# Optimization experiments

Hardware: AMD Instinct MI355X
Metric: run time of the kernel (lower is better)

Reference implementation:

```python
import jax, jax.numpy as jnp
import numpy as np

THRESHOLD = 2.0 / 3.0


def _quantize_1_58_bit(weight):
    """BitNet b1.58: ternary {-1,0,+1} * scale, scale = mean(|w|) clamped."""
    scale = jnp.clip(jnp.mean(jnp.abs(weight)), 1e-5, 1000.0)
    weight_norm = jnp.clip(weight / scale, -10.0, 10.0)
    q = jnp.where(weight_norm > THRESHOLD, 1.0,
                  jnp.where(weight_norm < -THRESHOLD, -1.0, 0.0)).astype(weight.dtype)
    return q, scale


def setup_inputs() -> dict:
    key = jax.random.key(0)
    k1, k2 = jax.random.split(key)
    B, S, D_IN, D_OUT = 4, 2048, 4096, 4096
    x = jax.random.normal(k1, (B, S, D_IN), dtype=jnp.float32)
    weight = jax.random.normal(k2, (D_OUT, D_IN), dtype=jnp.float32)
    bias = jnp.zeros((D_OUT,), dtype=jnp.float32)
    return {"x": x, "weight": weight, "bias": bias}


def reference(x, weight, bias):
    # Training-path forward value == eval-path forward value:
    # dequantized ternary weight, F.linear semantics (x @ W.T + b).
    q, scale = _quantize_1_58_bit(weight)
    weight_q = q * scale  # [out, in]
    out = jnp.einsum('bsi,oi->bso', x, weight_q) + bias
    return out
```

## Files before the change

kernel.cpp:

```cpp
#include <hip/hip_runtime.h>
#include <hip/hip_bf16.h>
#include <stdint.h>


#define BM 128
#define BN 128
#define BK 64

typedef __bf16 bf16x8 __attribute__((ext_vector_type(8)));
typedef float f32x4 __attribute__((ext_vector_type(4)));
typedef unsigned short u16x8 __attribute__((ext_vector_type(8)));

__device__ __forceinline__ unsigned short f2bf_rne(float f) {
  union { float f; unsigned int u; } v; v.f = f;
  unsigned int u = v.u;
  u += 0x7FFFu + ((u >> 16) & 1u);
  return (unsigned short)(u >> 16);
}

__global__ void absum_kernel(const float4* __restrict__ w, int n4,
                             double* __restrict__ out) {
  float s = 0.f;
  for (int i = blockIdx.x * blockDim.x + threadIdx.x; i < n4;
       i += gridDim.x * blockDim.x) {
    float4 v = w[i];
    s += fabsf(v.x) + fabsf(v.y) + fabsf(v.z) + fabsf(v.w);
  }
#pragma unroll
  for (int off = 32; off > 0; off >>= 1) s += __shfl_down(s, off);
  __shared__ float partial[4];
  if ((threadIdx.x & 63) == 0) partial[threadIdx.x >> 6] = s;
  __syncthreads();
  if (threadIdx.x == 0)
    atomicAdd(out, (double)(partial[0] + partial[1] + partial[2] + partial[3]));
}

__global__ void quant_kernel(const float4* __restrict__ w, int n8,
                             const double* __restrict__ sum, double inv_cnt,
                             u16x8* __restrict__ q) {
  float scale = (float)fmin(fmax(sum[0] * inv_cnt, 1e-5), 1000.0);
  const float T = 2.0f / 3.0f;
  for (int i = blockIdx.x * blockDim.x + threadIdx.x; i < n8;
       i += gridDim.x * blockDim.x) {
    float4 a = w[2 * i], b = w[2 * i + 1];
    float f[8] = {a.x, a.y, a.z, a.w, b.x, b.y, b.z, b.w};
    u16x8 o;
#pragma unroll
    for (int j = 0; j < 8; ++j) {
      float n = f[j] / scale;
      o[j] = (n > T) ? 0x3F80u : ((n < -T) ? 0xBF80u : 0u);
    }
    q[i] = o;
  }
}

__global__ void xcvt_kernel(const float4* __restrict__ x, int n8,
                            u16x8* __restrict__ xb) {
  for (int i = blockIdx.x * blockDim.x + threadIdx.x; i < n8;
       i += gridDim.x * blockDim.x) {
    float4 a = x[2 * i], b = x[2 * i + 1];
    float f[8] = {a.x, a.y, a.z, a.w, b.x, b.y, b.z, b.w};
    u16x8 o;
#pragma unroll
    for (int j = 0; j < 8; ++j) o[j] = f2bf_rne(f[j]);
    xb[i] = o;
  }
}

__global__ void gemm_kernel(const ushort* __restrict__ xb,
                            const ushort* __restrict__ qb,
                            const float* __restrict__ bias,
                            const double* __restrict__ sum,
                            float* __restrict__ out,
                            int M, int N, int K, double inv_cnt) {
  __shared__ __align__(16) ushort As[BM * BK];
  __shared__ __align__(16) ushort Bs[BN * BK];

  const int t = threadIdx.x;
  const int wave = t >> 6;
  const int lane = t & 63;
  const int m0 = blockIdx.y * BM;
  const int n0 = blockIdx.x * BN;

  const int wr = (wave >> 1) * 64;
  const int wc = (wave & 1) * 64;
  const int lm = lane & 15;
  const int lk = lane >> 4;

  const int srow = lane >> 3;
  const int schunk = (lane & 7) ^ srow;
  const ushort* ag = xb + (size_t)(m0 + wave * 32 + srow) * K + schunk * 8;
  const ushort* bg = qb + (size_t)(n0 + wave * 32 + srow) * K + schunk * 8;
  ushort* al = &As[(wave * 32) * BK];
  ushort* bl = &Bs[(wave * 32) * BK];

  f32x4 acc[4][4] = {};

  for (int k0 = 0; k0 < K; k0 += BK) {
#pragma unroll
    for (int s = 0; s < 4; ++s) {
      __builtin_amdgcn_global_load_lds(
          (const __attribute__((address_space(1))) void*)(ag + (size_t)s * 8 * K),
          (__attribute__((address_space(3))) void*)(al + s * 8 * BK), 16, 0, 0);
      __builtin_amdgcn_global_load_lds(
          (const __attribute__((address_space(1))) void*)(bg + (size_t)s * 8 * K),
          (__attribute__((address_space(3))) void*)(bl + s * 8 * BK), 16, 0, 0);
    }
    __syncthreads();

#pragma unroll
    for (int ks = 0; ks < 2; ++ks) {
      bf16x8 af[4], bf[4];
#pragma unroll
      for (int i = 0; i < 4; ++i) {
        const int row = wr + i * 16 + lm;
        const int slot = (ks * 4 + lk) ^ (lm & 7);
        af[i] = *(const bf16x8*)&As[row * BK + slot * 8];
      }
#pragma unroll
      for (int j = 0; j < 4; ++j) {
        const int row = wc + j * 16 + lm;
        const int slot = (ks * 4 + lk) ^ (lm & 7);
        bf[j] = *(const bf16x8*)&Bs[row * BK + slot * 8];
      }
#pragma unroll
      for (int i = 0; i < 4; ++i)
#pragma unroll
        for (int j = 0; j < 4; ++j)
          acc[i][j] = __builtin_amdgcn_mfma_f32_16x16x32_bf16(af[i], bf[j],
                                                             acc[i][j], 0, 0, 0);
    }
    __syncthreads();
    ag += BK;
    bg += BK;
  }

  float scale = (float)fmin(fmax(sum[0] * inv_cnt, 1e-5), 1000.0);

#pragma unroll
  for (int j = 0; j < 4; ++j) {
    const int col = n0 + wc + j * 16 + lm;
    const float bv = bias[col];
#pragma unroll
    for (int i = 0; i < 4; ++i) {
      const int row = m0 + wr + i * 16 + lk * 4;
      float* op = out + (size_t)row * N + col;
#pragma unroll
      for (int r = 0; r < 4; ++r)
        op[(size_t)r * N] = acc[i][j][r] * scale + bv;
    }
  }
}

extern "C" void kernel_launch(void* const* d_in, const int* in_sizes, int n_in,
                              void* d_out, int out_size, void* d_ws,
                              size_t ws_size, hipStream_t stream) {
  const float* x = (const float*)d_in[0];
  const float* w = (const float*)d_in[1];
  const float* bias = (const float*)d_in[2];
  float* out = (float*)d_out;

  const int DOUT = in_sizes[2];
  const int DIN = in_sizes[1] / DOUT;
  const int M = in_sizes[0] / DIN;
  const int N = DOUT, K = DIN;

  char* ws = (char*)d_ws;
  double* sum = (double*)ws;
  ushort* xb = (ushort*)(ws + 256);
  ushort* qb = (ushort*)(ws + 256 + (size_t)M * K * 2);

  const double inv_cnt = 1.0 / ((double)N * (double)K);

  hipMemsetAsync(d_ws, 0, 8, stream);

  const int wn4 = (N * K) / 4;
  const int wn8 = (N * K) / 8;
  absum_kernel<<<2048, 256, 0, stream>>>((const float4*)w, wn4, sum);
  quant_kernel<<<4096, 256, 0, stream>>>((const float4*)w, wn8, sum, inv_cnt,
                                         (u16x8*)qb);
  const int xn8 = (M * K) / 8;
  xcvt_kernel<<<8192, 256, 0, stream>>>((const float4*)x, xn8, (u16x8*)xb);

  dim3 grid(N / BN, M / BM);
  gemm_kernel<<<grid, 256, 0, stream>>>(xb, qb, bias, sum, out, M, N, K,
                                        inv_cnt);
}
```

Baseline: 542.6 us.

## Rewrite GEMM as 256x256 tile, 8-wave, double-buffered ping-pong pipeline

Replaces the 128x128 single-buffered GEMM with a 256x256 block tile using 512 threads (8 waves, 2x4 layout, each wave computing 128x64). LDS is double-buffered in halves, and the next k-tile's global-to-LDS loads are interleaved with MFMA quadrants using explicit barriers, vmcnt/lgkmcnt waits and s_setprio. A grid swizzle remaps block IDs so that nearby blocks share tiles in L2. The aim is to hide global-load latency and raise arithmetic intensity, in exchange for 128KB of LDS, heavy register pressure (128 accumulator floats per thread) and fragile hand-written synchronization.

```diff
diff --git a/kernel.cpp b/kernel.cpp
--- a/kernel.cpp
+++ b/kernel.cpp
@@ -2,10 +2,6 @@
 #include <hip/hip_bf16.h>
 #include <stdint.h>
 
-
-#define BM 128
-#define BN 128
-#define BK 64
 
 typedef __bf16 bf16x8 __attribute__((ext_vector_type(8)));
 typedef float f32x4 __attribute__((ext_vector_type(4)));
@@ -67,87 +63,170 @@
   }
 }
 
-__global__ void gemm_kernel(const ushort* __restrict__ xb,
-                            const ushort* __restrict__ qb,
-                            const float* __restrict__ bias,
-                            const double* __restrict__ sum,
-                            float* __restrict__ out,
-                            int M, int N, int K, double inv_cnt) {
-  __shared__ __align__(16) ushort As[BM * BK];
-  __shared__ __align__(16) ushort Bs[BN * BK];
+
+#define BKT 64
+
+#define FENCE() asm volatile("" ::: "memory")
+#define BAR() __builtin_amdgcn_s_barrier()
+#define WAIT_LGKM0() asm volatile("s_waitcnt lgkmcnt(0)" ::: "memory")
+#define WAIT_VM4() asm volatile("s_waitcnt vmcnt(4)" ::: "memory")
+
+__global__ __launch_bounds__(512, 2)
+void gemm_kernel(const ushort* __restrict__ xb,
+                 const ushort* __restrict__ qb,
+                 const float* __restrict__ bias,
+                 const double* __restrict__ sum,
+                 float* __restrict__ out,
+                 int M, int N, int K, double inv_cnt) {
+  __shared__ __align__(16) ushort As[2][2][128][64];
+  __shared__ __align__(16) ushort Bs[2][2][128][64];
 
   const int t = threadIdx.x;
-  const int wave = t >> 6;
+  const int w = t >> 6;
   const int lane = t & 63;
-  const int m0 = blockIdx.y * BM;
-  const int n0 = blockIdx.x * BN;
-
-  const int wr = (wave >> 1) * 64;
-  const int wc = (wave & 1) * 64;
+  const int wm = w >> 2;
+  const int wn = w & 3;
   const int lm = lane & 15;
   const int lk = lane >> 4;
 
+  const int nbx = N >> 8;
+  const int cpx = gridDim.x >> 3;
+  const int id = blockIdx.x;
+  const int swz = (id & 7) * cpx + (id >> 3);
+  const int bx = swz % nbx;
+  const int by = swz / nbx;
+  const int m0 = by << 8;
+  const int n0 = bx << 8;
+
   const int srow = lane >> 3;
   const int schunk = (lane & 7) ^ srow;
-  const ushort* ag = xb + (size_t)(m0 + wave * 32 + srow) * K + schunk * 8;
-  const ushort* bg = qb + (size_t)(n0 + wave * 32 + srow) * K + schunk * 8;
-  ushort* al = &As[(wave * 32) * BK];
-  ushort* bl = &Bs[(wave * 32) * BK];
-
-  f32x4 acc[4][4] = {};
-
-  for (int k0 = 0; k0 < K; k0 += BK) {
-#pragma unroll
-    for (int s = 0; s < 4; ++s) {
-      __builtin_amdgcn_global_load_lds(
-          (const __attribute__((address_space(1))) void*)(ag + (size_t)s * 8 * K),
-          (__attribute__((address_space(3))) void*)(al + s * 8 * BK), 16, 0, 0);
-      __builtin_amdgcn_global_load_lds(
-          (const __attribute__((address_space(1))) void*)(bg + (size_t)s * 8 * K),
-          (__attribute__((address_space(3))) void*)(bl + s * 8 * BK), 16, 0, 0);
-    }
-    __syncthreads();
-
-#pragma unroll
-    for (int ks = 0; ks < 2; ++ks) {
-      bf16x8 af[4], bf[4];
-#pragma unroll
-      for (int i = 0; i < 4; ++i) {
-        const int row = wr + i * 16 + lm;
-        const int slot = (ks * 4 + lk) ^ (lm & 7);
-        af[i] = *(const bf16x8*)&As[row * BK + slot * 8];
-      }
-#pragma unroll
-      for (int j = 0; j < 4; ++j) {
-        const int row = wc + j * 16 + lm;
-        const int slot = (ks * 4 + lk) ^ (lm & 7);
-        bf[j] = *(const bf16x8*)&Bs[row * BK + slot * 8];
-      }
-#pragma unroll
-      for (int i = 0; i < 4; ++i)
-#pragma unroll
-        for (int j = 0; j < 4; ++j)
-          acc[i][j] = __builtin_amdgcn_mfma_f32_16x16x32_bf16(af[i], bf[j],
-                                                             acc[i][j], 0, 0, 0);
-    }
-    __syncthreads();
-    ag += BK;
-    bg += BK;
+  const ushort* aSrc = xb + (size_t)(m0 + w * 8 + srow) * K + schunk * 8;
+  const ushort* bSrc = qb + (size_t)(n0 + w * 8 + srow) * K + schunk * 8;
+
+#define STAGE_A(BUF, H, KT)                                                    \
+  do {                                                                         \
+    _Pragma("unroll") for (int s_ = 0; s_ < 2; ++s_) {                         \
+      __builtin_amdgcn_global_load_lds(                                        \
+          (const __attribute__((address_space(1))) void*)(                     \
+              aSrc + (size_t)((H) * 128 + s_ * 64) * K + (KT) * BKT),          \
+          (__attribute__((address_space(3))) void*)(                           \
+              &As[BUF][H][s_ * 64 + w * 8][0]),                                \
+          16, 0, 0);                                                           \
+    }                                                                          \
+  } while (0)
+
+#define STAGE_B(BUF, H, KT)                                                    \
+  do {                                                                         \
+    _Pragma("unroll") for (int s_ = 0; s_ < 2; ++s_) {                         \
+      __builtin_amdgcn_global_load_lds(                                        \
+          (const __attribute__((address_space(1))) void*)(                     \
+              bSrc + (size_t)((H) * 128 + s_ * 64) * K + (KT) * BKT),          \
+          (__attribute__((address_space(3))) void*)(                           \
+              &Bs[BUF][H][s_ * 64 + w * 8][0]),                                \
+          16, 0, 0);                                                           \
+    }                                                                          \
+  } while (0)
+
+#define RD_A(BUF, MH)                                                          \
+  _Pragma("unroll") for (int mq = 0; mq < 4; ++mq)                             \
+  _Pragma("unroll") for (int ks = 0; ks < 2; ++ks)                             \
+      af[mq][ks] = *(const bf16x8*)&As[BUF][wm][(MH) * 64 + mq * 16 + lm]      \
+                                      [((ks * 4 + lk) ^ (lm & 7)) * 8];
+
+#define RD_B(BUF, NF0)                                                         \
+  _Pragma("unroll") for (int nf = (NF0); nf < (NF0) + 2; ++nf)                 \
+  _Pragma("unroll") for (int ks = 0; ks < 2; ++ks)                             \
+      bf[nf][ks] =                                                             \
+          *(const bf16x8*)&Bs[BUF][wn >> 1][(wn & 1) * 64 + nf * 16 + lm]      \
+                              [((ks * 4 + lk) ^ (lm & 7)) * 8];
+
+#define MFMA_Q(MH, NB)                                                         \
+  _Pragma("unroll") for (int mq = 0; mq < 4; ++mq)                             \
+  _Pragma("unroll") for (int nq = 0; nq < 2; ++nq)                             \
+  _Pragma("unroll") for (int ks = 0; ks < 2; ++ks)                             \
+      acc[(MH) * 4 + mq][(NB) + nq] =                                          \
+          __builtin_amdgcn_mfma_f32_16x16x32_bf16(                             \
+              af[mq][ks], bf[(NB) + nq][ks], acc[(MH) * 4 + mq][(NB) + nq],    \
+              0, 0, 0);
+
+  f32x4 acc[8][4] = {};
+  bf16x8 af[4][2];
+  bf16x8 bf[4][2];
+
+  STAGE_A(0, 0, 0); STAGE_A(0, 1, 0);
+  STAGE_B(0, 0, 0); STAGE_B(0, 1, 0);
+  STAGE_B(1, 0, 1); STAGE_B(1, 1, 1);
+  WAIT_VM4();
+  FENCE(); BAR(); FENCE();
+
+  const int NT = K / BKT;
+  for (int i = 0; i < NT / 2; ++i) {
+    const int kt1 = 2 * i + 1;
+    const int kt2 = (2 * i + 2 < NT) ? (2 * i + 2) : (NT - 1);
+    const int kt3 = (2 * i + 3 < NT) ? (2 * i + 3) : (NT - 1);
+
+    RD_A(0, 0); RD_B(0, 0);
+    STAGE_A(1, 0, kt1);
+    FENCE(); BAR(); WAIT_LGKM0();
+    __builtin_amdgcn_s_setprio(1); MFMA_Q(0, 0); __builtin_amdgcn_s_setprio(0);
+    FENCE(); BAR();
+
+    RD_B(0, 2);
+    STAGE_A(1, 1, kt1);
+    FENCE(); BAR(); WAIT_LGKM0();
+    __builtin_amdgcn_s_setprio(1); MFMA_Q(0, 2); __builtin_amdgcn_s_setprio(0);
+    FENCE(); BAR();
+
+    RD_A(0, 1);
+    STAGE_B(0, 0, kt2);
+    FENCE(); BAR(); WAIT_LGKM0();
+    __builtin_amdgcn_s_setprio(1); MFMA_Q(1, 2); __builtin_amdgcn_s_setprio(0);
+    FENCE(); BAR();
+
+    STAGE_B(0, 1, kt2);
+    FENCE(); BAR();
+    __builtin_amdgcn_s_setprio(1); MFMA_Q(1, 0); __builtin_amdgcn_s_setprio(0);
+    WAIT_VM4();
+    FENCE(); BAR();
+
+    RD_A(1, 0); RD_B(1, 0);
+    STAGE_A(0, 0, kt2);
+    FENCE(); BAR(); WAIT_LGKM0();
+    __builtin_amdgcn_s_setprio(1); MFMA_Q(0, 0); __builtin_amdgcn_s_setprio(0);
+    FENCE(); BAR();
+
+    RD_B(1, 2);
+    STAGE_A(0, 1, kt2);
+    FENCE(); BAR(); WAIT_LGKM0();
+    __builtin_amdgcn_s_setprio(1); MFMA_Q(0, 2); __builtin_amdgcn_s_setprio(0);
+    FENCE(); BAR();
+
+    RD_A(1, 1);
+    STAGE_B(1, 0, kt3);
+    FENCE(); BAR(); WAIT_LGKM0();
+    __builtin_amdgcn_s_setprio(1); MFMA_Q(1, 2); __builtin_amdgcn_s_setprio(0);
+    FENCE(); BAR();
+
+    STAGE_B(1, 1, kt3);
+    FENCE(); BAR();
+    __builtin_amdgcn_s_setprio(1); MFMA_Q(1, 0); __builtin_amdgcn_s_setprio(0);
+    WAIT_VM4();
+    FENCE(); BAR();
   }
 
   float scale = (float)fmin(fmax(sum[0] * inv_cnt, 1e-5), 1000.0);
 
 #pragma unroll
-  for (int j = 0; j < 4; ++j) {
-    const int col = n0 + wc + j * 16 + lm;
+  for (int nf = 0; nf < 4; ++nf) {
+    const int col = n0 + wn * 64 + nf * 16 + lm;
     const float bv = bias[col];
 #pragma unroll
-    for (int i = 0; i < 4; ++i) {
-      const int row = m0 + wr + i * 16 + lk * 4;
+    for (int mf = 0; mf < 8; ++mf) {
+      const int row = m0 + wm * 128 + mf * 16 + lk * 4;
       float* op = out + (size_t)row * N + col;
 #pragma unroll
       for (int r = 0; r < 4; ++r)
-        op[(size_t)r * N] = acc[i][j][r] * scale + bv;
+        op[(size_t)r * N] = acc[mf][nf][r] * scale + bv;
     }
   }
 }
@@ -182,7 +261,7 @@
   const int xn8 = (M * K) / 8;
   xcvt_kernel<<<8192, 256, 0, stream>>>((const float4*)x, xn8, (u16x8*)xb);
 
-  dim3 grid(N / BN, M / BM);
-  gemm_kernel<<<grid, 256, 0, stream>>>(xb, qb, bias, sum, out, M, N, K,
-                                        inv_cnt);
-}
+  const int nwg = (M >> 8) * (N >> 8);
+  gemm_kernel<<<dim3(nwg), 512, 0, stream>>>(xb, qb, bias, sum, out, M, N, K,
+                                             inv_cnt);
+}
```

New measurement: 616.8 us. 1.14x slower.
